# Performance work log

Measured on AMD Instinct MI355X. Metric: run time of the kernel, lower is better.

Reference implementation:

```python
import jax, jax.numpy as jnp
import numpy as np

B = 262144      # batch
DIN = 100       # input covariate dim (cfg_density[0][0])
H = 64          # hidden dim
G = 10          # num_grid -> density output dim G+1
NH = 5          # number of dosage-bucket heads in Multi_head


def setup_inputs() -> dict:
    key = jax.random.key(0)
    ks = jax.random.split(key, 16)
    s = 0.05
    return {
        "dosage": jax.random.uniform(ks[0], (B,), dtype=jnp.float32),
        "x": jax.random.normal(ks[1], (B, DIN), dtype=jnp.float32),
        # density feature MLP (two Linear+ReLU layers)
        "dW0": jax.random.normal(ks[2], (DIN, H), dtype=jnp.float32) * s,
        "db0": jax.random.normal(ks[3], (H,), dtype=jnp.float32) * s,
        "dW1": jax.random.normal(ks[4], (H, H), dtype=jnp.float32) * s,
        "db1": jax.random.normal(ks[5], (H,), dtype=jnp.float32) * s,
        # Density_Block: Linear(H -> G+1) then softmax + grid interpolation
        "dbW": jax.random.normal(ks[6], (H, G + 1), dtype=jnp.float32) * s,
        "dbB": jax.random.normal(ks[7], (G + 1,), dtype=jnp.float32) * s,
        # Multi_head: 5 structurally identical heads, params stacked on axis 0
        # layer0: Treat_Linear(64 -> 64, relu, istreat=1)
        "W0": jax.random.normal(ks[8], (NH, H, H), dtype=jnp.float32) * s,
        "tw0": jax.random.normal(ks[9], (NH, H), dtype=jnp.float32) * s,
        "b0": jax.random.normal(ks[10], (NH, H), dtype=jnp.float32) * s,
        # layer1 (last): Treat_Linear(64 -> 1, no act, istreat=1)
        "W1": jax.random.normal(ks[11], (NH, H, 1), dtype=jnp.float32) * s,
        "tw1": jax.random.normal(ks[12], (NH, 1), dtype=jnp.float32) * s,
        "b1": jax.random.normal(ks[13], (NH, 1), dtype=jnp.float32) * s,
    }


def reference(dosage, x, dW0, db0, dW1, db1, dbW, dbB, W0, tw0, b0, W1, tw1, b1):
    # hidden feature MLP
    hidden = jax.nn.relu(x @ dW0 + db0)
    hidden = jax.nn.relu(hidden @ dW1 + db1)            # [B, H]

    # ---- Density_Block: softmax over grid, dual gather + linear interpolation
    p = jax.nn.softmax(hidden @ dbW + dbB, axis=1)      # [B, G+1]
    tB = dosage * G
    U = jnp.ceil(tB)
    inter = 1.0 - (U - tB)                              # fractional position in cell
    Ui = U.astype(jnp.int32)
    Li = Ui - 1
    Li = Li + (Li < 0).astype(jnp.int32)                # clamp L=-1 -> 0
    pL = jnp.take_along_axis(p, Li[:, None], axis=1)[:, 0]
    pU = jnp.take_along_axis(p, Ui[:, None], axis=1)[:, 0]
    g = pL + (pU - pL) * inter                          # [B]

    # ---- Multi_head: 5 heads on dosage buckets [0,.2),[.2,.4),...,[.8,1.)
    t = dosage
    # layer0: out = feat @ W + t * tw + b, relu; compute all heads, select later
    h0 = jax.nn.relu(
        jnp.einsum('bi,hio->bho', hidden, W0)
        + t[:, None, None] * tw0[None]
        + b0[None]
    )                                                   # [B, NH, H]
    # last layer: no activation
    out1 = (jnp.einsum('bho,hoj->bhj', h0, W1)
            + t[:, None, None] * tw1[None]
            + b1[None])                                 # [B, NH, 1]
    bucket = jnp.clip(jnp.floor(t * NH).astype(jnp.int32), 0, NH - 1)
    Q = jnp.take_along_axis(out1, bucket[:, None, None], axis=1)[:, 0, :]  # [B, 1]
    return g, Q
```

## Files before the change

kernel.cpp:

```cpp
#include <hip/hip_runtime.h>

typedef __attribute__((ext_vector_type(8))) short  short8;
typedef __attribute__((ext_vector_type(4))) float  floatx4;
typedef __attribute__((ext_vector_type(4))) int    intx4;

constexpr int DIN = 100;
constexpr int H   = 64;
constexpr int G   = 10;
constexpr int NH  = 5;
constexpr int MWG = 128;
constexpr int HP  = 72;
constexpr int PBP = 20;

constexpr int NF_DW0 = 16, NF_DW1 = 8, NF_DBW = 2;
constexpr int NF_LIN = NF_DW0 + NF_DW1 + NF_DBW;
constexpr int NF_TOT = NF_LIN + 40;

__device__ __forceinline__ unsigned short f2bf_rne(float f) {
    union { float f; unsigned u; } v{f};
    unsigned r = v.u + 0x7FFF + ((v.u >> 16) & 1);
    return (unsigned short)(r >> 16);
}

__device__ __forceinline__ short8 pack8(const float* f) {
    intx4 p;
    #pragma unroll
    for (int j = 0; j < 4; ++j) {
        unsigned a = __float_as_uint(f[2 * j])     + 0x8000u;
        unsigned b = __float_as_uint(f[2 * j + 1]) + 0x8000u;
        p[j] = (int)((b & 0xFFFF0000u) | (a >> 16));
    }
    union { intx4 i; short8 s; } u; u.i = p;
    return u.s;
}

__device__ __forceinline__ unsigned pack2bf(float a, float b) {
    unsigned ua = __float_as_uint(a) + 0x8000u;
    unsigned ub = __float_as_uint(b) + 0x8000u;
    return (ua >> 16) | (ub & 0xFFFF0000u);
}

__device__ __forceinline__ short8 ldfrag(const unsigned short* __restrict__ ws,
                                         int f, int lane) {
    return *(const short8*)(ws + (size_t)(f * 64 + lane) * 8);
}

__global__ __launch_bounds__(64) void pack_kernel(
    const float* __restrict__ dW0, const float* __restrict__ dW1,
    const float* __restrict__ dbW, const float* __restrict__ W0,
    unsigned short* __restrict__ ws)
{
    const int f = blockIdx.x;
    const int lane = threadIdx.x;
    const int q = lane >> 4, cl = lane & 15;
    float v[8];
    if (f < NF_DW0) {
        int c = f >> 2, g = f & 3;
        #pragma unroll
        for (int j = 0; j < 8; ++j) {
            int k = c * 32 + q * 8 + j, n = g * 16 + cl;
            v[j] = (k < DIN) ? dW0[k * H + n] : 0.0f;
        }
    } else if (f < NF_DW0 + NF_DW1) {
        int r = f - NF_DW0; int c = r >> 2, g = r & 3;
        #pragma unroll
        for (int j = 0; j < 8; ++j) {
            int k = c * 32 + q * 8 + j, n = g * 16 + cl;
            v[j] = dW1[k * H + n];
        }
    } else if (f < NF_LIN) {
        int c = f - (NF_DW0 + NF_DW1);
        #pragma unroll
        for (int j = 0; j < 8; ++j) {
            int k = c * 32 + q * 8 + j, n = cl;
            v[j] = (n <= G) ? dbW[k * (G + 1) + n] : 0.0f;
        }
    } else {
        int r = f - NF_LIN; int h = r >> 3; r &= 7; int c = r >> 2, g = r & 3;
        #pragma unroll
        for (int j = 0; j < 8; ++j) {
            int k = c * 32 + q * 8 + j, n = g * 16 + cl;
            v[j] = W0[(h * H + k) * H + n];
        }
    }
    short8 s;
    #pragma unroll
    for (int j = 0; j < 8; ++j) s[j] = (short)f2bf_rne(v[j]);
    *(short8*)(ws + (size_t)(f * 64 + lane) * 8) = s;
}

__global__ __launch_bounds__(256, 4) void drnet_mfma(
    const float* __restrict__ dosage, const float* __restrict__ x,
    const float* __restrict__ db0, const float* __restrict__ db1,
    const float* __restrict__ dbB,
    const float* __restrict__ tw0, const float* __restrict__ b0,
    const float* __restrict__ W1, const float* __restrict__ tw1,
    const float* __restrict__ b1,
    const unsigned short* __restrict__ wsfrag,
    float* __restrict__ outg, float* __restrict__ outq)
{
    __shared__ unsigned short hbuf[4][32 * HP];
    __shared__ float          pbuf[4][16][PBP];
    __shared__ int            perm[4][32];
    __shared__ float          tbufs[4][32];
    __shared__ int            bks[4][32];
    __shared__ float          qbufs[4][32];

    const int tid  = threadIdx.x;
    const int wave = tid >> 6, lane = tid & 63;
    const int q = lane >> 4, cl = lane & 15;
    const int rowbase = blockIdx.x * MWG + wave * 32;
    unsigned short* hb = hbuf[wave];

    floatx4 xv[2][7];
    #pragma unroll
    for (int mt = 0; mt < 2; ++mt) {
        const float* xr = x + (size_t)(rowbase + mt * 16 + cl) * DIN;
        #pragma unroll
        for (int cch = 0; cch < 3; ++cch) {
            xv[mt][2 * cch]     = *(const floatx4*)(xr + cch * 32 + q * 8);
            xv[mt][2 * cch + 1] = *(const floatx4*)(xr + cch * 32 + q * 8 + 4);
        }
        xv[mt][6] = (q == 0) ? *(const floatx4*)(xr + 96) : (floatx4)0.0f;
    }

    {
        const int row = lane & 31;
        const float tl = dosage[rowbase + row];
        int bk = (int)floorf(tl * (float)NH);
        bk = min(max(bk, 0), NH - 1);
        const unsigned m0 = (unsigned)__ballot(bk == 0);
        const unsigned m1 = (unsigned)__ballot(bk == 1);
        const unsigned m2 = (unsigned)__ballot(bk == 2);
        const unsigned m3 = (unsigned)__ballot(bk == 3);
        const unsigned m4 = (unsigned)__ballot(bk == 4);
        int base = 0;
        base += (bk > 0) ? __popc(m0) : 0;
        base += (bk > 1) ? __popc(m1) : 0;
        base += (bk > 2) ? __popc(m2) : 0;
        base += (bk > 3) ? __popc(m3) : 0;
        const unsigned mymask = (bk == 0) ? m0 : (bk == 1) ? m1 :
                                (bk == 2) ? m2 : (bk == 3) ? m3 : m4;
        const int pos = base + __popc(mymask & ((1u << row) - 1u));
        if (lane < 32) {
            perm[wave][pos]  = row;
            tbufs[wave][pos] = tl;
            bks[wave][pos]   = bk;
        }
    }

    {
        short8 a1[2][4];
        #pragma unroll
        for (int mt = 0; mt < 2; ++mt)
            #pragma unroll
            for (int cch = 0; cch < 4; ++cch) {
                float f[8];
                if (cch < 3) {
                    #pragma unroll
                    for (int j = 0; j < 4; ++j) {
                        f[j]     = xv[mt][2 * cch][j];
                        f[4 + j] = xv[mt][2 * cch + 1][j];
                    }
                } else {
                    #pragma unroll
                    for (int j = 0; j < 4; ++j) {
                        f[j]     = xv[mt][6][j];
                        f[4 + j] = 0.0f;
                    }
                }
                a1[mt][cch] = pack8(f);
            }
        floatx4 acc[2][4];
        #pragma unroll
        for (int mt = 0; mt < 2; ++mt)
            #pragma unroll
            for (int g = 0; g < 4; ++g) acc[mt][g] = (floatx4)0.0f;
        #pragma unroll
        for (int cch = 0; cch < 4; ++cch)
            #pragma unroll
            for (int g = 0; g < 4; ++g) {
                short8 bf = ldfrag(wsfrag, cch * 4 + g, lane);
                acc[0][g] = __builtin_amdgcn_mfma_f32_16x16x32_bf16(bf, a1[0][cch], acc[0][g], 0, 0, 0);
                acc[1][g] = __builtin_amdgcn_mfma_f32_16x16x32_bf16(bf, a1[1][cch], acc[1][g], 0, 0, 0);
            }
        #pragma unroll
        for (int mt = 0; mt < 2; ++mt)
            #pragma unroll
            for (int g = 0; g < 4; ++g) {
                floatx4 bias = *(const floatx4*)(db0 + g * 16 + 4 * q);
                float v0 = fmaxf(acc[mt][g][0] + bias[0], 0.0f);
                float v1 = fmaxf(acc[mt][g][1] + bias[1], 0.0f);
                float v2 = fmaxf(acc[mt][g][2] + bias[2], 0.0f);
                float v3 = fmaxf(acc[mt][g][3] + bias[3], 0.0f);
                *(uint2*)(hb + (size_t)(mt * 16 + cl) * HP + g * 16 + 4 * q) =
                    make_uint2(pack2bf(v0, v1), pack2bf(v2, v3));
            }
    }

    {
        short8 a2[2][2];
        #pragma unroll
        for (int mt = 0; mt < 2; ++mt)
            #pragma unroll
            for (int cch = 0; cch < 2; ++cch)
                a2[mt][cch] = *(const short8*)(hb + (mt * 16 + cl) * HP + cch * 32 + q * 8);
        floatx4 acc[2][4];
        #pragma unroll
        for (int mt = 0; mt < 2; ++mt)
            #pragma unroll
            for (int g = 0; g < 4; ++g) acc[mt][g] = (floatx4)0.0f;
        #pragma unroll
        for (int cch = 0; cch < 2; ++cch)
            #pragma unroll
            for (int g = 0; g < 4; ++g) {
                short8 bf = ldfrag(wsfrag, NF_DW0 + cch * 4 + g, lane);
                acc[0][g] = __builtin_amdgcn_mfma_f32_16x16x32_bf16(bf, a2[0][cch], acc[0][g], 0, 0, 0);
                acc[1][g] = __builtin_amdgcn_mfma_f32_16x16x32_bf16(bf, a2[1][cch], acc[1][g], 0, 0, 0);
            }
        #pragma unroll
        for (int mt = 0; mt < 2; ++mt)
            #pragma unroll
            for (int g = 0; g < 4; ++g) {
                floatx4 bias = *(const floatx4*)(db1 + g * 16 + 4 * q);
                float v0 = fmaxf(acc[mt][g][0] + bias[0], 0.0f);
                float v1 = fmaxf(acc[mt][g][1] + bias[1], 0.0f);
                float v2 = fmaxf(acc[mt][g][2] + bias[2], 0.0f);
                float v3 = fmaxf(acc[mt][g][3] + bias[3], 0.0f);
                *(uint2*)(hb + (size_t)(mt * 16 + cl) * HP + g * 16 + 4 * q) =
                    make_uint2(pack2bf(v0, v1), pack2bf(v2, v3));
            }
    }

    {
        float tden[2];
        #pragma unroll
        for (int mt = 0; mt < 2; ++mt)
            tden[mt] = dosage[rowbase + mt * 16 + cl];
        short8 af[2][2];
        #pragma unroll
        for (int mt = 0; mt < 2; ++mt)
            #pragma unroll
            for (int cch = 0; cch < 2; ++cch)
                af[mt][cch] = *(const short8*)(hb + (mt * 16 + cl) * HP + cch * 32 + q * 8);
        floatx4 accd[2];
        accd[0] = (floatx4)0.0f; accd[1] = (floatx4)0.0f;
        #pragma unroll
        for (int cch = 0; cch < 2; ++cch) {
            short8 bf = ldfrag(wsfrag, NF_DW0 + NF_DW1 + cch, lane);
            #pragma unroll
            for (int mt = 0; mt < 2; ++mt)
                accd[mt] = __builtin_amdgcn_mfma_f32_16x16x32_bf16(bf, af[mt][cch], accd[mt], 0, 0, 0);
        }
        #pragma unroll
        for (int mt = 0; mt < 2; ++mt) {
            floatx4 ev;
            float sp = 0.0f;
            #pragma unroll
            for (int r = 0; r < 4; ++r) {
                const int gd = 4 * q + r;
                float e = (gd <= G) ? __expf(accd[mt][r] + dbB[gd]) : 0.0f;
                ev[r] = e;
                sp += e;
            }
            float s = sp;
            s += __shfl_xor(s, 16); s += __shfl_xor(s, 32);
            *(floatx4*)(&pbuf[wave][cl][4 * q]) = ev;
            const float tt = tden[mt];
            const float tB = tt * (float)G;
            const float U  = ceilf(tB);
            const float inter = 1.0f - (U - tB);
            int Ui = (int)U; int Li = Ui - 1; if (Li < 0) Li = 0;
            const float pL = pbuf[wave][cl][Li];
            const float pU = pbuf[wave][cl][Ui];
            if (q == 0)
                outg[rowbase + mt * 16 + cl] = (pL + (pU - pL) * inter) / s;
        }
    }

    {
        short8 ag[2][2];
        int    prow[2], bkme[2], blo[2], bhi[2];
        float  tme[2];
        #pragma unroll
        for (int mt = 0; mt < 2; ++mt) {
            const int base = mt * 16;
            prow[mt] = perm[wave][base + cl];
            ag[mt][0] = *(const short8*)(hb + prow[mt] * HP + q * 8);
            ag[mt][1] = *(const short8*)(hb + prow[mt] * HP + 32 + q * 8);
            tme[mt]  = tbufs[wave][base + cl];
            bkme[mt] = bks[wave][base + cl];
            blo[mt]  = bks[wave][base];
            bhi[mt]  = bks[wave][base + 15];
        }
        #pragma unroll
        for (int mt = 0; mt < 2; ++mt) {
            float qp = 0.0f;
            #pragma unroll 1
            for (int h = blo[mt]; h <= bhi[mt]; ++h) {
                floatx4 acch[4];
                #pragma unroll
                for (int g = 0; g < 4; ++g) acch[g] = (floatx4)0.0f;
                #pragma unroll
                for (int cch = 0; cch < 2; ++cch)
                    #pragma unroll
                    for (int g = 0; g < 4; ++g) {
                        short8 bf = ldfrag(wsfrag, NF_LIN + h * 8 + cch * 4 + g, lane);
                        acch[g] = __builtin_amdgcn_mfma_f32_16x16x32_bf16(bf, ag[mt][cch], acch[g], 0, 0, 0);
                    }
                if (bkme[mt] == h) {
                    #pragma unroll
                    for (int g = 0; g < 4; ++g) {
                        const int off = h * H + g * 16 + 4 * q;
                        floatx4 tw0v = *(const floatx4*)(tw0 + off);
                        floatx4 b0v  = *(const floatx4*)(b0  + off);
                        floatx4 w1v  = *(const floatx4*)(W1  + off);
                        #pragma unroll
                        for (int r = 0; r < 4; ++r)
                            qp += fmaxf(acch[g][r] + tme[mt] * tw0v[r] + b0v[r], 0.0f) * w1v[r];
                    }
                }
            }
            qp += __shfl_xor(qp, 16); qp += __shfl_xor(qp, 32);
            if (q == 0)
                qbufs[wave][prow[mt]] = qp + tme[mt] * tw1[bkme[mt]] + b1[bkme[mt]];
        }
    }

    if (lane < 8) {
        floatx4 v = *(const floatx4*)(&qbufs[wave][lane * 4]);
        *(floatx4*)(outq + rowbase + lane * 4) = v;
    }
}

extern "C" void kernel_launch(void* const* d_in, const int* in_sizes, int n_in,
                              void* d_out, int out_size, void* d_ws, size_t ws_size,
                              hipStream_t stream) {
    const float* dosage = (const float*)d_in[0];
    const float* x      = (const float*)d_in[1];
    const float* dW0    = (const float*)d_in[2];
    const float* db0    = (const float*)d_in[3];
    const float* dW1    = (const float*)d_in[4];
    const float* db1    = (const float*)d_in[5];
    const float* dbW    = (const float*)d_in[6];
    const float* dbB    = (const float*)d_in[7];
    const float* W0     = (const float*)d_in[8];
    const float* tw0    = (const float*)d_in[9];
    const float* b0     = (const float*)d_in[10];
    const float* W1     = (const float*)d_in[11];
    const float* tw1    = (const float*)d_in[12];
    const float* b1     = (const float*)d_in[13];

    const int Btot = in_sizes[0];
    float* outg = (float*)d_out;
    float* outq = outg + Btot;
    unsigned short* ws = (unsigned short*)d_ws;

    pack_kernel<<<NF_TOT, 64, 0, stream>>>(dW0, dW1, dbW, W0, ws);
    drnet_mfma<<<Btot / MWG, 256, 0, stream>>>(dosage, x, db0, db1, dbB,
                                               tw0, b0, W1, tw1, b1,
                                               ws, outg, outq);
}
```

Before: 211.2 us.

## Stage weight fragments in LDS, transpose activations via shuffles, run all heads unsorted

```diff
diff --git a/kernel.cpp b/kernel.cpp
--- a/kernel.cpp
+++ b/kernel.cpp
@@ -9,7 +9,6 @@
 constexpr int G   = 10;
 constexpr int NH  = 5;
 constexpr int MWG = 128;
-constexpr int HP  = 72;
 constexpr int PBP = 20;
 
 constexpr int NF_DW0 = 16, NF_DW1 = 8, NF_DBW = 2;
@@ -34,15 +33,10 @@
     return u.s;
 }
 
-__device__ __forceinline__ unsigned pack2bf(float a, float b) {
-    unsigned ua = __float_as_uint(a) + 0x8000u;
-    unsigned ub = __float_as_uint(b) + 0x8000u;
-    return (ua >> 16) | (ub & 0xFFFF0000u);
-}
-
-__device__ __forceinline__ short8 ldfrag(const unsigned short* __restrict__ ws,
-                                         int f, int lane) {
-    return *(const short8*)(ws + (size_t)(f * 64 + lane) * 8);
+__device__ __forceinline__ void bar_vm() {
+    asm volatile("s_waitcnt vmcnt(0) lgkmcnt(0)" ::: "memory");
+    __builtin_amdgcn_s_barrier();
+    asm volatile("" ::: "memory");
 }
 
 __global__ __launch_bounds__(64) void pack_kernel(
@@ -89,7 +83,7 @@
     *(short8*)(ws + (size_t)(f * 64 + lane) * 8) = s;
 }
 
-__global__ __launch_bounds__(256, 4) void drnet_mfma(
+__global__ __launch_bounds__(256, 2) void drnet_mfma(
     const float* __restrict__ dosage, const float* __restrict__ x,
     const float* __restrict__ db0, const float* __restrict__ db1,
     const float* __restrict__ dbB,
@@ -99,19 +93,48 @@
     const unsigned short* __restrict__ wsfrag,
     float* __restrict__ outg, float* __restrict__ outq)
 {
-    __shared__ unsigned short hbuf[4][32 * HP];
+    __shared__ unsigned short wstage[NF_TOT * 512];
     __shared__ float          pbuf[4][16][PBP];
-    __shared__ int            perm[4][32];
-    __shared__ float          tbufs[4][32];
-    __shared__ int            bks[4][32];
-    __shared__ float          qbufs[4][32];
 
     const int tid  = threadIdx.x;
     const int wave = tid >> 6, lane = tid & 63;
     const int q = lane >> 4, cl = lane & 15;
     const int rowbase = blockIdx.x * MWG + wave * 32;
-    unsigned short* hb = hbuf[wave];
-
+
+    auto ldsfrag = [&](int f) -> short8 {
+        return *(const short8*)(wstage + f * 512 + lane * 8);
+    };
+
+    auto xpose = [&](const floatx4 plo, const floatx4 phi) -> short8 {
+        float f[8];
+        const int sbase = ((q & 1) * 2) * 16 + cl;
+        #pragma unroll
+        for (int jj = 0; jj < 8; ++jj) {
+            const int srcl = sbase + ((jj >> 2) << 4);
+            const float vlo = __shfl(plo[jj & 3], srcl);
+            const float vhi = __shfl(phi[jj & 3], srcl);
+            f[jj] = (q >> 1) ? vhi : vlo;
+        }
+        return pack8(f);
+    };
+
+    #pragma unroll
+    for (int f0 = 0; f0 < 68; f0 += 4) {
+        const int f = f0 + wave;
+        if (f < NF_TOT) {
+            __builtin_amdgcn_global_load_lds(
+                (const __attribute__((address_space(1))) void*)
+                    (wsfrag + (size_t)(f * 64 + lane) * 8),
+                (__attribute__((address_space(3))) void*)
+                    (wstage + f * 512),
+                16, 0, 0);
+        }
+    }
+
+    float tden[2];
+    #pragma unroll
+    for (int mt = 0; mt < 2; ++mt)
+        tden[mt] = dosage[rowbase + mt * 16 + cl];
     floatx4 xv[2][7];
     #pragma unroll
     for (int mt = 0; mt < 2; ++mt) {
@@ -124,31 +147,9 @@
         xv[mt][6] = (q == 0) ? *(const floatx4*)(xr + 96) : (floatx4)0.0f;
     }
 
-    {
-        const int row = lane & 31;
-        const float tl = dosage[rowbase + row];
-        int bk = (int)floorf(tl * (float)NH);
-        bk = min(max(bk, 0), NH - 1);
-        const unsigned m0 = (unsigned)__ballot(bk == 0);
-        const unsigned m1 = (unsigned)__ballot(bk == 1);
-        const unsigned m2 = (unsigned)__ballot(bk == 2);
-        const unsigned m3 = (unsigned)__ballot(bk == 3);
-        const unsigned m4 = (unsigned)__ballot(bk == 4);
-        int base = 0;
-        base += (bk > 0) ? __popc(m0) : 0;
-        base += (bk > 1) ? __popc(m1) : 0;
-        base += (bk > 2) ? __popc(m2) : 0;
-        base += (bk > 3) ? __popc(m3) : 0;
-        const unsigned mymask = (bk == 0) ? m0 : (bk == 1) ? m1 :
-                                (bk == 2) ? m2 : (bk == 3) ? m3 : m4;
-        const int pos = base + __popc(mymask & ((1u << row) - 1u));
-        if (lane < 32) {
-            perm[wave][pos]  = row;
-            tbufs[wave][pos] = tl;
-            bks[wave][pos]   = bk;
-        }
-    }
-
+    bar_vm();
+
+    short8 a2[2][2];
     {
         short8 a1[2][4];
         #pragma unroll
@@ -180,74 +181,61 @@
         for (int cch = 0; cch < 4; ++cch)
             #pragma unroll
             for (int g = 0; g < 4; ++g) {
-                short8 bf = ldfrag(wsfrag, cch * 4 + g, lane);
+                short8 bf = ldsfrag(cch * 4 + g);
                 acc[0][g] = __builtin_amdgcn_mfma_f32_16x16x32_bf16(bf, a1[0][cch], acc[0][g], 0, 0, 0);
                 acc[1][g] = __builtin_amdgcn_mfma_f32_16x16x32_bf16(bf, a1[1][cch], acc[1][g], 0, 0, 0);
             }
         #pragma unroll
-        for (int mt = 0; mt < 2; ++mt)
+        for (int mt = 0; mt < 2; ++mt) {
+            floatx4 pv[4];
             #pragma unroll
             for (int g = 0; g < 4; ++g) {
                 floatx4 bias = *(const floatx4*)(db0 + g * 16 + 4 * q);
-                float v0 = fmaxf(acc[mt][g][0] + bias[0], 0.0f);
-                float v1 = fmaxf(acc[mt][g][1] + bias[1], 0.0f);
-                float v2 = fmaxf(acc[mt][g][2] + bias[2], 0.0f);
-                float v3 = fmaxf(acc[mt][g][3] + bias[3], 0.0f);
-                *(uint2*)(hb + (size_t)(mt * 16 + cl) * HP + g * 16 + 4 * q) =
-                    make_uint2(pack2bf(v0, v1), pack2bf(v2, v3));
-            }
-    }
-
+                #pragma unroll
+                for (int r = 0; r < 4; ++r)
+                    pv[g][r] = fmaxf(acc[mt][g][r] + bias[r], 0.0f);
+            }
+            a2[mt][0] = xpose(pv[0], pv[1]);
+            a2[mt][1] = xpose(pv[2], pv[3]);
+        }
+    }
+
+    short8 af[2][2];
     {
-        short8 a2[2][2];
+        floatx4 acc[2][4];
         #pragma unroll
         for (int mt = 0; mt < 2; ++mt)
             #pragma unroll
-            for (int cch = 0; cch < 2; ++cch)
-                a2[mt][cch] = *(const short8*)(hb + (mt * 16 + cl) * HP + cch * 32 + q * 8);
-        floatx4 acc[2][4];
-        #pragma unroll
-        for (int mt = 0; mt < 2; ++mt)
-            #pragma unroll
             for (int g = 0; g < 4; ++g) acc[mt][g] = (floatx4)0.0f;
         #pragma unroll
         for (int cch = 0; cch < 2; ++cch)
             #pragma unroll
             for (int g = 0; g < 4; ++g) {
-                short8 bf = ldfrag(wsfrag, NF_DW0 + cch * 4 + g, lane);
+                short8 bf = ldsfrag(NF_DW0 + cch * 4 + g);
                 acc[0][g] = __builtin_amdgcn_mfma_f32_16x16x32_bf16(bf, a2[0][cch], acc[0][g], 0, 0, 0);
                 acc[1][g] = __builtin_amdgcn_mfma_f32_16x16x32_bf16(bf, a2[1][cch], acc[1][g], 0, 0, 0);
             }
         #pragma unroll
-        for (int mt = 0; mt < 2; ++mt)
+        for (int mt = 0; mt < 2; ++mt) {
+            floatx4 pv[4];
             #pragma unroll
             for (int g = 0; g < 4; ++g) {
                 floatx4 bias = *(const floatx4*)(db1 + g * 16 + 4 * q);
-                float v0 = fmaxf(acc[mt][g][0] + bias[0], 0.0f);
-                float v1 = fmaxf(acc[mt][g][1] + bias[1], 0.0f);
-                float v2 = fmaxf(acc[mt][g][2] + bias[2], 0.0f);
-                float v3 = fmaxf(acc[mt][g][3] + bias[3], 0.0f);
-                *(uint2*)(hb + (size_t)(mt * 16 + cl) * HP + g * 16 + 4 * q) =
-                    make_uint2(pack2bf(v0, v1), pack2bf(v2, v3));
-            }
+                #pragma unroll
+                for (int r = 0; r < 4; ++r)
+                    pv[g][r] = fmaxf(acc[mt][g][r] + bias[r], 0.0f);
+            }
+            af[mt][0] = xpose(pv[0], pv[1]);
+            af[mt][1] = xpose(pv[2], pv[3]);
+        }
     }
 
     {
-        float tden[2];
-        #pragma unroll
-        for (int mt = 0; mt < 2; ++mt)
-            tden[mt] = dosage[rowbase + mt * 16 + cl];
-        short8 af[2][2];
-        #pragma unroll
-        for (int mt = 0; mt < 2; ++mt)
-            #pragma unroll
-            for (int cch = 0; cch < 2; ++cch)
-                af[mt][cch] = *(const short8*)(hb + (mt * 16 + cl) * HP + cch * 32 + q * 8);
         floatx4 accd[2];
         accd[0] = (floatx4)0.0f; accd[1] = (floatx4)0.0f;
         #pragma unroll
         for (int cch = 0; cch < 2; ++cch) {
-            short8 bf = ldfrag(wsfrag, NF_DW0 + NF_DW1 + cch, lane);
+            short8 bf = ldsfrag(NF_DW0 + NF_DW1 + cch);
             #pragma unroll
             for (int mt = 0; mt < 2; ++mt)
                 accd[mt] = __builtin_amdgcn_mfma_f32_16x16x32_bf16(bf, af[mt][cch], accd[mt], 0, 0, 0);
@@ -279,35 +267,28 @@
     }
 
     {
-        short8 ag[2][2];
-        int    prow[2], bkme[2], blo[2], bhi[2];
-        float  tme[2];
-        #pragma unroll
-        for (int mt = 0; mt < 2; ++mt) {
-            const int base = mt * 16;
-            prow[mt] = perm[wave][base + cl];
-            ag[mt][0] = *(const short8*)(hb + prow[mt] * HP + q * 8);
-            ag[mt][1] = *(const short8*)(hb + prow[mt] * HP + 32 + q * 8);
-            tme[mt]  = tbufs[wave][base + cl];
-            bkme[mt] = bks[wave][base + cl];
-            blo[mt]  = bks[wave][base];
-            bhi[mt]  = bks[wave][base + 15];
-        }
-        #pragma unroll
-        for (int mt = 0; mt < 2; ++mt) {
-            float qp = 0.0f;
-            #pragma unroll 1
-            for (int h = blo[mt]; h <= bhi[mt]; ++h) {
-                floatx4 acch[4];
+        int bkme[2];
+        #pragma unroll
+        for (int mt = 0; mt < 2; ++mt)
+            bkme[mt] = min(max((int)floorf(tden[mt] * (float)NH), 0), NH - 1);
+        float qp[2] = {0.0f, 0.0f};
+        #pragma unroll 1
+        for (int h = 0; h < NH; ++h) {
+            floatx4 acch[2][4];
+            #pragma unroll
+            for (int mt = 0; mt < 2; ++mt)
                 #pragma unroll
-                for (int g = 0; g < 4; ++g) acch[g] = (floatx4)0.0f;
+                for (int g = 0; g < 4; ++g) acch[mt][g] = (floatx4)0.0f;
+            #pragma unroll
+            for (int cch = 0; cch < 2; ++cch)
                 #pragma unroll
-                for (int cch = 0; cch < 2; ++cch)
-                    #pragma unroll
-                    for (int g = 0; g < 4; ++g) {
-                        short8 bf = ldfrag(wsfrag, NF_LIN + h * 8 + cch * 4 + g, lane);
-                        acch[g] = __builtin_amdgcn_mfma_f32_16x16x32_bf16(bf, ag[mt][cch], acch[g], 0, 0, 0);
-                    }
+                for (int g = 0; g < 4; ++g) {
+                    short8 bf = ldsfrag(NF_LIN + h * 8 + cch * 4 + g);
+                    acch[0][g] = __builtin_amdgcn_mfma_f32_16x16x32_bf16(bf, af[0][cch], acch[0][g], 0, 0, 0);
+                    acch[1][g] = __builtin_amdgcn_mfma_f32_16x16x32_bf16(bf, af[1][cch], acch[1][g], 0, 0, 0);
+                }
+            #pragma unroll
+            for (int mt = 0; mt < 2; ++mt) {
                 if (bkme[mt] == h) {
                     #pragma unroll
                     for (int g = 0; g < 4; ++g) {
@@ -317,19 +298,19 @@
                         floatx4 w1v  = *(const floatx4*)(W1  + off);
                         #pragma unroll
                         for (int r = 0; r < 4; ++r)
-                            qp += fmaxf(acch[g][r] + tme[mt] * tw0v[r] + b0v[r], 0.0f) * w1v[r];
+                            qp[mt] += fmaxf(acch[mt][g][r] + tden[mt] * tw0v[r] + b0v[r], 0.0f) * w1v[r];
                     }
                 }
             }
-            qp += __shfl_xor(qp, 16); qp += __shfl_xor(qp, 32);
+        }
+        #pragma unroll
+        for (int mt = 0; mt < 2; ++mt) {
+            float s = qp[mt];
+            s += __shfl_xor(s, 16); s += __shfl_xor(s, 32);
             if (q == 0)
-                qbufs[wave][prow[mt]] = qp + tme[mt] * tw1[bkme[mt]] + b1[bkme[mt]];
-        }
-    }
-
-    if (lane < 8) {
-        floatx4 v = *(const floatx4*)(&qbufs[wave][lane * 4]);
-        *(floatx4*)(outq + rowbase + lane * 4) = v;
+                outq[rowbase + mt * 16 + cl] =
+                    s + tden[mt] * tw1[bkme[mt]] + b1[bkme[mt]];
+        }
     }
 }
 
```

Result: slower. 218.8 us (+3.6%).
